# Kernel optimization log

Measured on AMD Instinct MI355X. Metric: run time of the kernel, lower is better.

Reference implementation:

```python
import jax, jax.numpy as jnp
import numpy as np

SW, FB, EMB, H = 96, 64, 512, 3   # seg_width, freq_bandwidth, embedding_dim, num_heads
B, T = 4, 1024
F = SW * FB


def setup_inputs() -> dict:
    key = jax.random.key(0)
    ks = jax.random.split(key, 12)
    s = 0.02
    dh = SW // H
    return {
        "x": jax.random.normal(ks[0], (B, T, F), jnp.float32),
        "o_enc": jax.random.randint(ks[1], (B, T), 0, 2, jnp.int32),
        "r_enc": jax.random.normal(ks[2], (B, T, EMB), jnp.float32),
        "Wq": jax.random.normal(ks[3], (SW, SW), jnp.float32) * s,
        "bq": jnp.zeros((SW,), jnp.float32),
        "Wk": jax.random.normal(ks[4], (SW, SW), jnp.float32) * s,
        "bk": jnp.zeros((SW,), jnp.float32),
        "Wv": jax.random.normal(ks[5], (SW, SW), jnp.float32) * s,
        "bv": jnp.zeros((SW,), jnp.float32),
        "Er": jax.random.normal(ks[6], (FB, dh), jnp.float32) * s,   # relative pos embeddings, max_len = FB
        "W1": jax.random.normal(ks[7], (SW, 4 * SW), jnp.float32) * s,
        "b1": jnp.zeros((4 * SW,), jnp.float32),
        "W2": jax.random.normal(ks[8], (4 * SW, SW), jnp.float32) * s,
        "b2": jnp.zeros((SW,), jnp.float32),
        "We": jax.random.normal(ks[9], (F, EMB), jnp.float32) * s,
        "be": jnp.zeros((EMB,), jnp.float32),
    }


def _skew(qer):
    # qer: (N, h, L, L) -> Srel via Music-Transformer skewing
    padded = jnp.pad(qer, ((0, 0), (0, 0), (0, 0), (1, 0)))      # (N,h,L,L+1)
    n, h, l, l1 = padded.shape
    return padded.reshape(n, h, l1, l)[:, :, 1:, :]               # (N,h,L,L)


def _rel_attention(x, Wq, bq, Wk, bk, Wv, bv, Er):
    # x: (N, L, D); relative global self-attention with causal mask
    N, L, D = x.shape
    dh = D // H

    def heads(t):
        return t.reshape(N, L, H, dh).transpose(0, 2, 1, 3)       # (N,h,L,dh)

    q = heads(x @ Wq + bq)
    k = heads(x @ Wk + bk)
    v = heads(x @ Wv + bv)
    qer = jnp.einsum('nhld,md->nhlm', q, Er)                      # (N,h,L,L)
    srel = _skew(qer)
    scores = (jnp.einsum('nhld,nhmd->nhlm', q, k) + srel) / jnp.sqrt(jnp.asarray(dh, x.dtype))
    causal = jnp.triu(jnp.ones((L, L), bool), 1)
    scores = jnp.where(causal, jnp.finfo(scores.dtype).min, scores)
    attn = jax.nn.softmax(scores, axis=-1)
    out = jnp.einsum('nhlm,nhmd->nhld', attn, v)
    return out.transpose(0, 2, 1, 3).reshape(N, L, D)


def _segmentwise_mean(data, block_ids):
    # data: (B,T,E), block_ids: (B,T) contiguous non-decreasing segment ids in [0,T)
    Bn, Tn, En = data.shape
    seg_sum = jax.vmap(lambda d, i: jax.ops.segment_sum(d, i, num_segments=Tn))(data, block_ids)
    cnt = jax.vmap(lambda i: jax.ops.segment_sum(jnp.ones_like(i), i, num_segments=Tn))(block_ids)
    means = seg_sum / jnp.maximum(cnt, 1).astype(data.dtype)[..., None]
    is_start = jnp.concatenate(
        [jnp.ones((Bn, 1), bool), block_ids[:, 1:] != block_ids[:, :-1]], axis=1)
    gathered = jnp.take_along_axis(means, block_ids[..., None], axis=1)   # (B,T,E)
    # original writes each block's mean only at the block's first position, zeros elsewhere
    return jnp.where(is_start[..., None], gathered, jnp.zeros((), data.dtype))


def reference(x, o_enc, r_enc, Wq, bq, Wk, bk, Wv, bv, Er, W1, b1, W2, b2, We, be):
    Bn, Tn, Fn = x.shape
    xr = x.reshape(Bn * Tn, SW, FB).transpose(0, 2, 1)            # (B*T, FB, SW)
    emb = _rel_attention(xr, Wq, bq, Wk, bk, Wv, bv, Er)
    emb = jax.nn.relu(emb @ W1 + b1) @ W2 + b2                    # FFN: SW -> 4SW -> SW
    emb = emb.transpose(0, 2, 1).reshape(Bn, Tn, Fn)
    emb = emb @ We + be                                           # (B,T,EMB)
    # nn.LayerNorm(emb.shape): normalize over the WHOLE tensor, no affine, eps=1e-8
    mu = emb.mean()
    var = ((emb - mu) ** 2).mean()
    emb = (emb - mu) / jnp.sqrt(var + 1e-8)
    # _regionalize: block ids from cumsum of binary boundary indicators
    block_ids = jnp.cumsum(o_enc, axis=1)
    block_ids = block_ids - block_ids[:, :1]                      # matches 'if b[0]==1: b -= 1'
    block_means = _segmentwise_mean(emb, block_ids)
    return block_means + r_enc + emb
```

## Files before the change

### kernel.cpp

```cpp
#include <hip/hip_runtime.h>
#include <hip/hip_bf16.h>


typedef __attribute__((ext_vector_type(8))) short bf16x8;
typedef __attribute__((ext_vector_type(4))) float f32x4;

struct PtrTab { const void* p[16]; };

enum : int {
  O_WQT = 0,
  O_BQ  = 9984,
  O_WKT = 10080,
  O_BK  = 20064,
  O_WVT = 20160,
  O_BV  = 30144,
  O_ER  = 30240,
  O_W1T = 32288,
  O_B1  = 72224,
  O_W2C = 72608,
  O_B2  = 118688,
  O_WET = 118784
};

__device__ __forceinline__ float b2f(__hip_bfloat16 v) { return __bfloat162float(v); }
__device__ __forceinline__ __hip_bfloat16 f2b(float v) { return __float2bfloat16(v); }

__global__ __launch_bounds__(256) void prep_kernel(PtrTab tab,
                                                   __hip_bfloat16* __restrict__ Wc,
                                                   float* __restrict__ sums)
{
    __shared__ __hip_bfloat16 tile[64][65];
    const int bid = blockIdx.x, tid = threadIdx.x;
    const int kt = bid % 96, nt = bid / 96;
    const float* We = (const float*)tab.p[14];
    const int k0 = kt * 64, n0 = nt * 64;
    for (int e = tid; e < 4096; e += 256) {
        int kk = e >> 6, nn = e & 63;
        tile[nn][kk] = f2b(We[(size_t)(k0 + kk) * 512 + n0 + nn]);
    }
    __syncthreads();
    __hip_bfloat16* dstT = Wc + O_WET + ((size_t)nt * 96 + kt) * 4096;
    for (int e = tid; e < 4096; e += 256) dstT[e] = tile[e >> 6][e & 63];

    const int g = bid * 256 + tid;
    const int stride = gridDim.x * 256;
    const float* Wq = (const float*)tab.p[3];
    const float* bq = (const float*)tab.p[4];
    const float* Wk = (const float*)tab.p[5];
    const float* bk = (const float*)tab.p[6];
    const float* Wv = (const float*)tab.p[7];
    const float* bv = (const float*)tab.p[8];
    const float* Er = (const float*)tab.p[9];
    const float* W1 = (const float*)tab.p[10];
    const float* b1 = (const float*)tab.p[11];
    const float* W2 = (const float*)tab.p[12];
    const float* b2 = (const float*)tab.p[13];

    for (int t = 0; t < 3; ++t) {
        const float* W = (t == 0 ? Wq : t == 1 ? Wk : Wv);
        __hip_bfloat16* d = Wc + t * 10080;
        for (int i = g; i < 9984; i += stride) {
            int j = i / 104, c = i - j * 104;
            d[i] = (c < 96) ? f2b(W[c * 96 + j]) : f2b(0.0f);
        }
    }
    for (int i = g; i < 96; i += stride) {
        Wc[O_BQ + i] = f2b(bq[i]);
        Wc[O_BK + i] = f2b(bk[i]);
        Wc[O_BV + i] = f2b(bv[i]);
        Wc[O_B2 + i] = f2b(b2[i]);
    }
    for (int i = g; i < 2048; i += stride) Wc[O_ER + i] = f2b(Er[i]);
    for (int i = g; i < 39936; i += stride) {
        int j = i / 104, c = i - j * 104;
        Wc[O_W1T + i] = (c < 96) ? f2b(W1[c * 384 + j]) : f2b(0.0f);
    }
    for (int i = g; i < 384; i += stride) Wc[O_B1 + i] = f2b(b1[i]);
    for (int i = g; i < 46080; i += stride) {
        int kc = i / 3840, r = i - kc * 3840;
        int nn = r / 40, kk = r - nn * 40;
        Wc[O_W2C + i] = (kk < 32) ? f2b(W2[(kc * 32 + kk) * 96 + nn]) : f2b(0.0f);
    }
    if (g < 2) sums[g] = 0.f;
}

__global__ __launch_bounds__(256, 4) void attn_ffn_kernel(
    const float* __restrict__ x, const __hip_bfloat16* __restrict__ Wc,
    __hip_bfloat16* __restrict__ M)
{
    const int n = blockIdx.x, tid = threadIdx.x;
    const int w = tid >> 6, lane = tid & 63, quad = lane >> 4, ln = lane & 15;

    __shared__ __align__(16) char smem[40448];
    __hip_bfloat16* xs  = (__hip_bfloat16*)(smem);
    __hip_bfloat16* kS  = (__hip_bfloat16*)(smem + 13312);
    __hip_bfloat16* vT  = (__hip_bfloat16*)(smem + 26624);
    __hip_bfloat16* hid = (__hip_bfloat16*)(smem + 13312);

    const f32x4 z4 = {0.f, 0.f, 0.f, 0.f};
    const int rowb = 16 * w + quad * 4;

    {
        const float* xb = x + (size_t)n * 6144;
        const int sb = w * 24;
        for (int c = 0; c < 3; ++c) {
            float v[8];
            #pragma unroll
            for (int j = 0; j < 8; ++j) v[j] = xb[(sb + c * 8 + j) * 64 + lane];
            union { __hip_bfloat16 h[8]; bf16x8 v8; } pk;
            #pragma unroll
            for (int j = 0; j < 8; ++j) pk.h[j] = f2b(v[j]);
            *(bf16x8*)(xs + lane * 104 + sb + c * 8) = pk.v8;
        }
    }
    __syncthreads();

    bf16x8 af[3];
    #pragma unroll
    for (int ks = 0; ks < 3; ++ks)
        af[ks] = *(const bf16x8*)(xs + (16 * w + ln) * 104 + ks * 32 + quad * 8);

    bf16x8 aqr[3];

    for (int st = 0; st < 6; ++st) {
        const int t = st >> 1, half = st & 1;
        const __hip_bfloat16* wsrc = Wc + t * 10080 + half * 4992;
        bf16x8 wf[9];
        #pragma unroll
        for (int i = 0; i < 9; ++i)
            wf[i] = *(const bf16x8*)(wsrc + ((i % 3) * 16 + ln) * 104 + (i / 3) * 32 + quad * 8);
        f32x4 acc[3] = {z4, z4, z4};
        #pragma unroll
        for (int ks = 0; ks < 3; ++ks)
            #pragma unroll
            for (int ct = 0; ct < 3; ++ct)
                acc[ct] = __builtin_amdgcn_mfma_f32_16x16x32_bf16(af[ks], wf[ks * 3 + ct], acc[ct], 0, 0, 0);
        const int j0 = half * 48;
        const __hip_bfloat16* bt = Wc + 9984 + t * 10080;
        #pragma unroll
        for (int ct = 0; ct < 3; ++ct) {
            int col = j0 + ct * 16 + ln;
            float bb = b2f(bt[col]);
            if (t < 2) {
                #pragma unroll
                for (int r = 0; r < 4; ++r)
                    kS[(rowb + r) * 104 + col] = f2b(acc[ct][r] + bb);
            } else {
                union { __hip_bfloat16 h4[4]; uint2 u; } pk;
                #pragma unroll
                for (int r = 0; r < 4; ++r) pk.h4[r] = f2b(acc[ct][r] + bb);
                *(uint2*)(vT + col * 72 + rowb) = pk.u;
            }
        }
        if (t == 0 && half == 1) {
            #pragma unroll
            for (int h = 0; h < 3; ++h)
                aqr[h] = *(const bf16x8*)(kS + (16 * w + ln) * 104 + h * 32 + quad * 8);
        }
    }

    bf16x8 erf[4];
    #pragma unroll
    for (int tn = 0; tn < 4; ++tn)
        erf[tn] = *(const bf16x8*)(Wc + O_ER + (16 * tn + ln) * 32 + quad * 8);
    __syncthreads();

    __hip_bfloat16* S2 = xs + 32;
    const int ql = 16 * w + ln;
    const int sshift = 63 - ql;
    f32x4 oacc[3][2] = {{z4, z4}, {z4, z4}, {z4, z4}};

    #pragma unroll
    for (int h = 0; h < 3; ++h) {
        const int c0 = h * 32;
        bf16x8 aq = aqr[h];
        #pragma unroll
        for (int tn = 0; tn < 4; ++tn) {
            f32x4 q4 = __builtin_amdgcn_mfma_f32_16x16x32_bf16(erf[tn], aq, z4, 0, 0, 0);
            #pragma unroll
            for (int r = 0; r < 4; ++r) {
                int e = 16 * tn + 4 * quad + r;
                if (e >= sshift) S2[ql * 104 + (e - sshift)] = f2b(q4[r]);
            }
        }
        float sco[4][4];
        #pragma unroll
        for (int tn = 0; tn < 4; ++tn) {
            bf16x8 kf = *(const bf16x8*)(kS + (16 * tn + ln) * 104 + c0 + quad * 8);
            f32x4 s1 = __builtin_amdgcn_mfma_f32_16x16x32_bf16(kf, aq, z4, 0, 0, 0);
            #pragma unroll
            for (int r = 0; r < 4; ++r) sco[tn][r] = s1[r];
        }
        #pragma unroll
        for (int tn = 0; tn < 4; ++tn) {
            union { __hip_bfloat16 h4[4]; uint2 u; } sr;
            sr.u = *(const uint2*)(S2 + ql * 104 + 16 * tn + 4 * quad);
            #pragma unroll
            for (int r = 0; r < 4; ++r) {
                int m = 16 * tn + 4 * quad + r;
                sco[tn][r] = (m <= ql)
                    ? (sco[tn][r] + b2f(sr.h4[r])) * 0.17677669529663687f
                    : -3.0e38f;
            }
        }
        float mt[4];
        #pragma unroll
        for (int tn = 0; tn < 4; ++tn)
            mt[tn] = fmaxf(fmaxf(sco[tn][0], sco[tn][1]), fmaxf(sco[tn][2], sco[tn][3]));
        float mx = fmaxf(fmaxf(mt[0], mt[1]), fmaxf(mt[2], mt[3]));
        mx = fmaxf(mx, __shfl_xor(mx, 16, 64));
        mx = fmaxf(mx, __shfl_xor(mx, 32, 64));
        float st_[4];
        #pragma unroll
        for (int tn = 0; tn < 4; ++tn) {
            #pragma unroll
            for (int r = 0; r < 4; ++r) sco[tn][r] = __expf(sco[tn][r] - mx);
            st_[tn] = (sco[tn][0] + sco[tn][1]) + (sco[tn][2] + sco[tn][3]);
        }
        float sum = (st_[0] + st_[1]) + (st_[2] + st_[3]);
        sum += __shfl_xor(sum, 16, 64);
        sum += __shfl_xor(sum, 32, 64);
        const float inv = 1.0f / sum;
        #pragma unroll
        for (int tn = 0; tn < 4; ++tn) {
            union { __hip_bfloat16 h4[4]; uint2 u; } pk;
            #pragma unroll
            for (int r = 0; r < 4; ++r) pk.h4[r] = f2b(sco[tn][r] * inv);
            *(uint2*)(S2 + ql * 104 + 16 * tn + 4 * quad) = pk.u;
        }
        #pragma unroll
        for (int ks2 = 0; ks2 < 2; ++ks2) {
            bf16x8 pa = *(const bf16x8*)(S2 + ql * 104 + ks2 * 32 + quad * 8);
            #pragma unroll
            for (int t2 = 0; t2 < 2; ++t2) {
                bf16x8 vb = *(const bf16x8*)(vT + (c0 + 16 * t2 + ln) * 72 + ks2 * 32 + quad * 8);
                oacc[h][t2] = __builtin_amdgcn_mfma_f32_16x16x32_bf16(pa, vb, oacc[h][t2], 0, 0, 0);
            }
        }
    }
    #pragma unroll
    for (int h = 0; h < 3; ++h)
        #pragma unroll
        for (int t2 = 0; t2 < 2; ++t2)
            #pragma unroll
            for (int r = 0; r < 4; ++r)
                xs[(rowb + r) * 104 + h * 32 + 16 * t2 + ln] = f2b(oacc[h][t2][r]);
    __syncthreads();

    bf16x8 cf[3];
    #pragma unroll
    for (int ks = 0; ks < 3; ++ks)
        cf[ks] = *(const bf16x8*)(xs + (16 * w + ln) * 104 + ks * 32 + quad * 8);

    f32x4 acc2[6] = {z4, z4, z4, z4, z4, z4};
    for (int jh = 0; jh < 2; ++jh) {
        #pragma unroll
        for (int cc = 0; cc < 4; ++cc) {
            const __hip_bfloat16* wsrc = Wc + O_W1T + (size_t)(jh * 192 + cc * 48) * 104;
            f32x4 a1[3] = {z4, z4, z4};
            #pragma unroll
            for (int ks = 0; ks < 3; ++ks)
                #pragma unroll
                for (int ct = 0; ct < 3; ++ct) {
                    bf16x8 b = *(const bf16x8*)(wsrc + (ct * 16 + ln) * 104 + ks * 32 + quad * 8);
                    a1[ct] = __builtin_amdgcn_mfma_f32_16x16x32_bf16(cf[ks], b, a1[ct], 0, 0, 0);
                }
            #pragma unroll
            for (int ct = 0; ct < 3; ++ct) {
                int colg = jh * 192 + cc * 48 + ct * 16 + ln;
                int coll = cc * 48 + ct * 16 + ln;
                float bb = b2f(Wc[O_B1 + colg]);
                #pragma unroll
                for (int r = 0; r < 4; ++r)
                    hid[(rowb + r) * 200 + coll] = f2b(fmaxf(a1[ct][r] + bb, 0.f));
            }
        }
        #pragma unroll
        for (int kc = 0; kc < 6; ++kc) {
            const __hip_bfloat16* nb = Wc + O_W2C + (size_t)(jh * 6 + kc) * 3840;
            bf16x8 a = *(const bf16x8*)(hid + (16 * w + ln) * 200 + kc * 32 + quad * 8);
            #pragma unroll
            for (int ct = 0; ct < 6; ++ct) {
                bf16x8 wfr = *(const bf16x8*)(nb + (ct * 16 + ln) * 40 + quad * 8);
                acc2[ct] = __builtin_amdgcn_mfma_f32_16x16x32_bf16(a, wfr, acc2[ct], 0, 0, 0);
            }
        }
    }

    __hip_bfloat16* Mg = M + (size_t)n * 6144;
    #pragma unroll
    for (int ct = 0; ct < 6; ++ct) {
        int d = ct * 16 + ln;
        float bb = b2f(Wc[O_B2 + d]);
        union { __hip_bfloat16 h4[4]; uint2 u; } pk;
        #pragma unroll
        for (int r = 0; r < 4; ++r) pk.h4[r] = f2b(acc2[ct][r] + bb);
        *(uint2*)((char*)Mg + (size_t)(d * 64 + rowb) * 2) = pk.u;
    }
}

__global__ __launch_bounds__(256) void gemm_kernel(
    const __hip_bfloat16* __restrict__ A,
    const __hip_bfloat16* __restrict__ Wc,
    const float* __restrict__ be,
    float* __restrict__ Y,
    float* __restrict__ sums)
{
    __shared__ __align__(16) __hip_bfloat16 As[2][64 * 72];
    __shared__ __align__(16) __hip_bfloat16 Bs[2][64 * 72];
    const int row0 = blockIdx.x * 64, nt = blockIdx.y, col0 = nt * 64;
    const int tid = threadIdx.x;
    const int w = tid >> 6, lane = tid & 63, quad = lane >> 4, ln = lane & 15;
    const int r0 = tid >> 3, c0_ = (tid & 7) * 8;
    const int r1 = r0 + 32,  c1_ = c0_;
    const size_t abase0 = (size_t)(row0 + r0) * 6144 + c0_;
    const size_t abase1 = (size_t)(row0 + r1) * 6144 + c1_;
    const __hip_bfloat16* Bsrc = Wc + O_WET + (size_t)nt * 96 * 4096;
    const size_t bbase0 = (size_t)r0 * 64 + c0_;
    const size_t bbase1 = (size_t)r1 * 64 + c1_;

    const f32x4 z4 = {0.f, 0.f, 0.f, 0.f};
    f32x4 acc[4] = {z4, z4, z4, z4};

    bf16x8 pa0 = *(const bf16x8*)(A + abase0);
    bf16x8 pa1 = *(const bf16x8*)(A + abase1);
    bf16x8 pb0 = *(const bf16x8*)(Bsrc + bbase0);
    bf16x8 pb1 = *(const bf16x8*)(Bsrc + bbase1);
    *(bf16x8*)(&As[0][r0 * 72 + c0_]) = pa0;
    *(bf16x8*)(&As[0][r1 * 72 + c1_]) = pa1;
    *(bf16x8*)(&Bs[0][r0 * 72 + c0_]) = pb0;
    *(bf16x8*)(&Bs[0][r1 * 72 + c1_]) = pb1;
    __syncthreads();

    for (int kt = 0; kt < 96; ++kt) {
        const int cur = kt & 1;
        if (kt < 95) {
            pa0 = *(const bf16x8*)(A + abase0 + (kt + 1) * 64);
            pa1 = *(const bf16x8*)(A + abase1 + (kt + 1) * 64);
            pb0 = *(const bf16x8*)(Bsrc + (size_t)(kt + 1) * 4096 + bbase0);
            pb1 = *(const bf16x8*)(Bsrc + (size_t)(kt + 1) * 4096 + bbase1);
        }
        #pragma unroll
        for (int ks = 0; ks < 2; ++ks) {
            bf16x8 a = *(const bf16x8*)(&As[cur][(16 * w + ln) * 72 + ks * 32 + quad * 8]);
            #pragma unroll
            for (int tn = 0; tn < 4; ++tn) {
                bf16x8 b = *(const bf16x8*)(&Bs[cur][(16 * tn + ln) * 72 + ks * 32 + quad * 8]);
                acc[tn] = __builtin_amdgcn_mfma_f32_16x16x32_bf16(a, b, acc[tn], 0, 0, 0);
            }
        }
        if (kt < 95) {
            *(bf16x8*)(&As[cur ^ 1][r0 * 72 + c0_]) = pa0;
            *(bf16x8*)(&As[cur ^ 1][r1 * 72 + c1_]) = pa1;
            *(bf16x8*)(&Bs[cur ^ 1][r0 * 72 + c0_]) = pb0;
            *(bf16x8*)(&Bs[cur ^ 1][r1 * 72 + c1_]) = pb1;
        }
        __syncthreads();
    }
    float s = 0.f, s2 = 0.f;
    #pragma unroll
    for (int tn = 0; tn < 4; ++tn) {
        int col = col0 + 16 * tn + ln;
        float bb = be[col];
        #pragma unroll
        for (int r = 0; r < 4; ++r) {
            float v = acc[tn][r] + bb;
            Y[(size_t)(row0 + 16 * w + quad * 4 + r) * 512 + col] = v;
            s += v; s2 += v * v;
        }
    }
    #pragma unroll
    for (int off = 1; off < 64; off <<= 1) {
        s  += __shfl_xor(s, off, 64);
        s2 += __shfl_xor(s2, off, 64);
    }
    __shared__ float r1s[4], r2s[4];
    if (lane == 0) { r1s[w] = s; r2s[w] = s2; }
    __syncthreads();
    if (tid == 0) {
        atomicAdd(&sums[0], r1s[0] + r1s[1] + r1s[2] + r1s[3]);
        atomicAdd(&sums[1], r2s[0] + r2s[1] + r2s[2] + r2s[3]);
    }
}

__global__ __launch_bounds__(256) void segid_kernel(const int* __restrict__ o_enc,
                                                    int* __restrict__ bids) {
    __shared__ int ts[256];
    const int b = blockIdx.x, tid = threadIdx.x;
    const int* o = o_enc + b * 1024;
    int v0 = o[4 * tid], v1 = o[4 * tid + 1], v2 = o[4 * tid + 2], v3 = o[4 * tid + 3];
    int p0 = v0, p1 = p0 + v1, p2 = p1 + v2, p3 = p2 + v3;
    ts[tid] = p3;
    __syncthreads();
    for (int off = 1; off < 256; off <<= 1) {
        int mine = ts[tid];
        int add = (tid >= off) ? ts[tid - off] : 0;
        __syncthreads();
        ts[tid] = mine + add;
        __syncthreads();
    }
    const int excl = (tid > 0) ? ts[tid - 1] : 0;
    const int off0 = o[0];
    int* bid = bids + b * 1024;
    bid[4 * tid]     = excl + p0 - off0;
    bid[4 * tid + 1] = excl + p1 - off0;
    bid[4 * tid + 2] = excl + p2 - off0;
    bid[4 * tid + 3] = excl + p3 - off0;
}

__global__ __launch_bounds__(256) void final_kernel(
    const float* __restrict__ Y, const int* __restrict__ bids,
    const float* __restrict__ sums, const float* __restrict__ r_enc,
    float* __restrict__ out)
{
    const int bt = blockIdx.x;
    const int b = bt >> 10, t = bt & 1023;
    const float mu = sums[0] * (1.0f / 2097152.0f);
    const float var = sums[1] * (1.0f / 2097152.0f) - mu * mu;
    const float rstd = rsqrtf(var + 1e-8f);
    const int* bid = bids + b * 1024;
    const int my = bid[t];
    const bool is_start = (t == 0) || (bid[t - 1] != my);
    int t2 = t + 1;
    float invc = 0.f;
    if (is_start) {
        while (t2 < 1024 && bid[t2] == my) ++t2;
        invc = 1.0f / (float)(t2 - t);
    }
    for (int e = threadIdx.x; e < 512; e += 256) {
        const size_t base = (size_t)bt * 512 + e;
        float res = (Y[base] - mu) * rstd + r_enc[base];
        if (is_start) {
            float s = 0.f;
            for (int tt = t; tt < t2; ++tt)
                s += (Y[((size_t)(b * 1024 + tt)) * 512 + e] - mu) * rstd;
            res += s * invc;
        }
        out[base] = res;
    }
}

extern "C" void kernel_launch(void* const* d_in, const int* in_sizes, int n_in,
                              void* d_out, int out_size, void* d_ws, size_t ws_size,
                              hipStream_t stream) {
    PtrTab tab;
    for (int i = 0; i < 16; ++i) tab.p[i] = d_in[i];

    char* ws = (char*)d_ws;
    __hip_bfloat16* M  = (__hip_bfloat16*)ws;
    float* Y           = (float*)(ws + 50331648);
    float* sums        = (float*)(ws + 58720256);
    int*   bids        = (int*)(ws + 58720320);
    __hip_bfloat16* Wc = (__hip_bfloat16*)(ws + 58736768);

    prep_kernel<<<768, 256, 0, stream>>>(tab, Wc, sums);
    attn_ffn_kernel<<<4096, 256, 0, stream>>>((const float*)d_in[0], Wc, M);
    gemm_kernel<<<dim3(64, 8), 256, 0, stream>>>(M, Wc, (const float*)d_in[15], Y, sums);
    segid_kernel<<<4, 256, 0, stream>>>((const int*)d_in[1], bids);
    final_kernel<<<4096, 256, 0, stream>>>(Y, bids, sums, (const float*)d_in[2], (float*)d_out);
}
```

Measured before the change: 436.9 us.

## Software-pipeline weight loads in attention/FFN kernel with register prefetch and LDS staging

Prefetches the next QKV weight fragments into registers while the current MFMAs run, stages each W1 chunk through a new LDS buffer that is filled from register prefetches issued one chunk ahead, and double-buffers the W2 fragments across the k-loop. The goal is to hide global/L2 latency of the per-block weight reads behind compute. In exchange it raises register pressure, drops the occupancy hint from launch bounds, grows LDS by about 10KB and adds two block barriers per W1 chunk, all of which may reduce occupancy.

Result: faster. 383.3 us (-12.3%).

```diff
diff --git a/kernel.cpp b/kernel.cpp
--- a/kernel.cpp
+++ b/kernel.cpp
@@ -84,21 +84,27 @@
     if (g < 2) sums[g] = 0.f;
 }
 
-__global__ __launch_bounds__(256, 4) void attn_ffn_kernel(
+__global__ __launch_bounds__(256) void attn_ffn_kernel(
     const float* __restrict__ x, const __hip_bfloat16* __restrict__ Wc,
     __hip_bfloat16* __restrict__ M)
 {
     const int n = blockIdx.x, tid = threadIdx.x;
     const int w = tid >> 6, lane = tid & 63, quad = lane >> 4, ln = lane & 15;
 
-    __shared__ __align__(16) char smem[40448];
+    __shared__ __align__(16) char smem[50432];
     __hip_bfloat16* xs  = (__hip_bfloat16*)(smem);
-    __hip_bfloat16* kS  = (__hip_bfloat16*)(smem + 13312);
-    __hip_bfloat16* vT  = (__hip_bfloat16*)(smem + 26624);
-    __hip_bfloat16* hid = (__hip_bfloat16*)(smem + 13312);
+    __hip_bfloat16* wb  = (__hip_bfloat16*)(smem + 13312);
+    __hip_bfloat16* kS  = (__hip_bfloat16*)(smem + 23296);
+    __hip_bfloat16* vT  = (__hip_bfloat16*)(smem + 36608);
+    __hip_bfloat16* hid = (__hip_bfloat16*)(smem + 23296);
 
     const f32x4 z4 = {0.f, 0.f, 0.f, 0.f};
     const int rowb = 16 * w + quad * 4;
+
+    bf16x8 wf[9], wfn[9];
+    #pragma unroll
+    for (int i = 0; i < 9; ++i)
+        wf[i] = *(const bf16x8*)(Wc + O_WQT + ((i % 3) * 16 + ln) * 104 + (i / 3) * 32 + quad * 8);
 
     {
         const float* xb = x + (size_t)n * 6144;
@@ -124,11 +130,12 @@
 
     for (int st = 0; st < 6; ++st) {
         const int t = st >> 1, half = st & 1;
-        const __hip_bfloat16* wsrc = Wc + t * 10080 + half * 4992;
-        bf16x8 wf[9];
-        #pragma unroll
-        for (int i = 0; i < 9; ++i)
-            wf[i] = *(const bf16x8*)(wsrc + ((i % 3) * 16 + ln) * 104 + (i / 3) * 32 + quad * 8);
+        if (st < 5) {
+            const __hip_bfloat16* nb = Wc + ((st + 1) >> 1) * 10080 + ((st + 1) & 1) * 4992;
+            #pragma unroll
+            for (int i = 0; i < 9; ++i)
+                wfn[i] = *(const bf16x8*)(nb + ((i % 3) * 16 + ln) * 104 + (i / 3) * 32 + quad * 8);
+        }
         f32x4 acc[3] = {z4, z4, z4};
         #pragma unroll
         for (int ks = 0; ks < 3; ++ks)
@@ -157,6 +164,8 @@
             for (int h = 0; h < 3; ++h)
                 aqr[h] = *(const bf16x8*)(kS + (16 * w + ln) * 104 + h * 32 + quad * 8);
         }
+        #pragma unroll
+        for (int i = 0; i < 9; ++i) wf[i] = wfn[i];
     }
 
     bf16x8 erf[4];
@@ -164,6 +173,13 @@
     for (int tn = 0; tn < 4; ++tn)
         erf[tn] = *(const bf16x8*)(Wc + O_ER + (16 * tn + ln) * 32 + quad * 8);
     __syncthreads();
+
+    bf16x8 pf0, pf1, pf2;
+    {
+        const bf16x8* src = (const bf16x8*)(Wc + O_W1T);
+        pf0 = src[tid]; pf1 = src[tid + 256];
+        if (tid + 512 < 624) pf2 = src[tid + 512];
+    }
 
     __hip_bfloat16* S2 = xs + 32;
     const int ql = 16 * w + ln;
@@ -253,21 +269,40 @@
         cf[ks] = *(const bf16x8*)(xs + (16 * w + ln) * 104 + ks * 32 + quad * 8);
 
     f32x4 acc2[6] = {z4, z4, z4, z4, z4, z4};
+    bf16x8 w2f[6], w2fn[6];
     for (int jh = 0; jh < 2; ++jh) {
-        #pragma unroll
         for (int cc = 0; cc < 4; ++cc) {
-            const __hip_bfloat16* wsrc = Wc + O_W1T + (size_t)(jh * 192 + cc * 48) * 104;
+            const int j0g = jh * 192 + cc * 48;
+            __syncthreads();
+            {
+                bf16x8* dst = (bf16x8*)wb;
+                dst[tid] = pf0;
+                dst[tid + 256] = pf1;
+                if (tid + 512 < 624) dst[tid + 512] = pf2;
+                if (cc < 3) {
+                    const bf16x8* src = (const bf16x8*)(Wc + O_W1T + jh * 19968 + (cc + 1) * 4992);
+                    pf0 = src[tid]; pf1 = src[tid + 256];
+                    if (tid + 512 < 624) pf2 = src[tid + 512];
+                } else {
+                    const __hip_bfloat16* nb = Wc + O_W2C + (jh * 6) * 3840;
+                    #pragma unroll
+                    for (int ct = 0; ct < 6; ++ct)
+                        w2f[ct] = *(const bf16x8*)(nb + (ct * 16 + ln) * 40 + quad * 8);
+                }
+            }
+            __syncthreads();
             f32x4 a1[3] = {z4, z4, z4};
             #pragma unroll
-            for (int ks = 0; ks < 3; ++ks)
+            for (int ks = 0; ks < 3; ++ks) {
                 #pragma unroll
                 for (int ct = 0; ct < 3; ++ct) {
-                    bf16x8 b = *(const bf16x8*)(wsrc + (ct * 16 + ln) * 104 + ks * 32 + quad * 8);
+                    bf16x8 b = *(const bf16x8*)(wb + (ct * 16 + ln) * 104 + ks * 32 + quad * 8);
                     a1[ct] = __builtin_amdgcn_mfma_f32_16x16x32_bf16(cf[ks], b, a1[ct], 0, 0, 0);
                 }
+            }
             #pragma unroll
             for (int ct = 0; ct < 3; ++ct) {
-                int colg = jh * 192 + cc * 48 + ct * 16 + ln;
+                int colg = j0g + ct * 16 + ln;
                 int coll = cc * 48 + ct * 16 + ln;
                 float bb = b2f(Wc[O_B1 + colg]);
                 #pragma unroll
@@ -275,14 +310,24 @@
                     hid[(rowb + r) * 200 + coll] = f2b(fmaxf(a1[ct][r] + bb, 0.f));
             }
         }
-        #pragma unroll
         for (int kc = 0; kc < 6; ++kc) {
-            const __hip_bfloat16* nb = Wc + O_W2C + (size_t)(jh * 6 + kc) * 3840;
+            if (kc < 5) {
+                const __hip_bfloat16* nb = Wc + O_W2C + (jh * 6 + kc + 1) * 3840;
+                #pragma unroll
+                for (int ct = 0; ct < 6; ++ct)
+                    w2fn[ct] = *(const bf16x8*)(nb + (ct * 16 + ln) * 40 + quad * 8);
+            } else if (jh == 0) {
+                const bf16x8* src = (const bf16x8*)(Wc + O_W1T + 19968);
+                pf0 = src[tid]; pf1 = src[tid + 256];
+                if (tid + 512 < 624) pf2 = src[tid + 512];
+            }
             bf16x8 a = *(const bf16x8*)(hid + (16 * w + ln) * 200 + kc * 32 + quad * 8);
             #pragma unroll
-            for (int ct = 0; ct < 6; ++ct) {
-                bf16x8 wfr = *(const bf16x8*)(nb + (ct * 16 + ln) * 40 + quad * 8);
-                acc2[ct] = __builtin_amdgcn_mfma_f32_16x16x32_bf16(a, wfr, acc2[ct], 0, 0, 0);
+            for (int ct = 0; ct < 6; ++ct)
+                acc2[ct] = __builtin_amdgcn_mfma_f32_16x16x32_bf16(a, w2f[ct], acc2[ct], 0, 0, 0);
+            if (kc < 5) {
+                #pragma unroll
+                for (int ct = 0; ct < 6; ++ct) w2f[ct] = w2fn[ct];
             }
         }
     }
```
